# Kernel tuning notes

Hardware: AMD Instinct MI355X
Metric: run time of the kernel (lower is better)

The kernel has to match this reference:

```python
import jax, jax.numpy as jnp
import numpy as np

B, D, K = 512, 128, 131072
TEMP = 0.07
PTR = 0  # queue_ptr starts at 0; B <= K so single contiguous write


def _normalize(x, axis):
    return x / jnp.linalg.norm(x, axis=axis, keepdims=True)


def setup_inputs() -> dict:
    key = jax.random.key(0)
    k = jax.random.split(key, 7)
    return {
        "predict0": jax.random.normal(k[0], (B, D), jnp.float32),
        "predict1": jax.random.normal(k[1], (B, D), jnp.float32),
        "project0": jax.random.normal(k[2], (B, D), jnp.float32),
        "project1": jax.random.normal(k[3], (B, D), jnp.float32),
        "queue": jax.random.normal(k[4], (D, K), jnp.float32),
        "queue_id": jax.random.randint(k[5], (K,), 0, 100000, jnp.int64) if jax.config.jax_enable_x64 else jax.random.randint(k[5], (K,), 0, 100000, jnp.int32),
        "ids": jax.random.randint(k[6], (B,), 0, 100000, jnp.int64) if jax.config.jax_enable_x64 else jax.random.randint(k[6], (B,), 0, 100000, jnp.int32),
    }


def _find_nn(proj, queue_n, queue_id, ids):
    # [B, K] similarity, mask out entries with same sample id, argmax, gather cols
    sim = proj @ queue_n                                   # [B, K]
    is_own = queue_id[None, :] == ids[:, None]             # [B, K]
    sim = jnp.where(is_own, jnp.float32(-1.0), sim)
    idx = jnp.argmax(sim, axis=1)                          # [B]
    return queue_n[:, idx]                                 # [D, B]


def _nnclr_loss(predicted, nn, temperature):
    # logits[i, j] = nn_i . predicted_j / T ; labels = arange(B)
    logits = (nn.T @ predicted.T) / temperature            # [B, B]
    logp = jax.nn.log_softmax(logits, axis=-1)
    return -jnp.mean(jnp.diagonal(logp))


def reference(predict0, predict1, project0, project1, queue, queue_id, ids):
    # forward_encoder's normalization (encoder itself is external and modeled out)
    p0 = _normalize(predict0, 1)
    p1 = _normalize(predict1, 1)
    z0 = _normalize(project0, 1)
    z1 = _normalize(project1, 1)
    queue_n = _normalize(queue, 0)  # queue stored normalized along dim 0

    # find_nn / queue are no_grad in the original
    nn0 = jax.lax.stop_gradient(_find_nn(jax.lax.stop_gradient(z0), queue_n, queue_id, ids))
    nn1 = jax.lax.stop_gradient(_find_nn(jax.lax.stop_gradient(z1), queue_n, queue_id, ids))

    loss0 = _nnclr_loss(p0, nn1, TEMP)
    loss1 = _nnclr_loss(p1, nn0, TEMP)
    loss = (loss0 + loss1) * 0.5

    # _dequeue_and_enqueue: ptr=0, B <= K -> contiguous slice write
    new_queue = jax.lax.dynamic_update_slice(queue_n, jax.lax.stop_gradient(z0.T), (0, PTR))
    new_queue_id = jax.lax.dynamic_update_slice(queue_id, ids, (PTR,))
    new_ptr = jnp.array((PTR + B) % K, dtype=queue_id.dtype)
    return loss, new_queue, new_queue_id, new_ptr
```

## Files before the change

### kernel.cpp

```cpp
#include <hip/hip_runtime.h>
#include <hip/hip_bf16.h>

typedef _Float16 half8 __attribute__((ext_vector_type(8)));
typedef _Float16 half4 __attribute__((ext_vector_type(4)));
typedef float f32x4 __attribute__((ext_vector_type(4)));

#define B 512
#define D 128
#define K 131072
#define TEMP 0.07f
#define NKB 256
#define KT_PER 32
#define NSS 16

#define INVN_OFF 0
#define Z0_OFF   131072
#define Z1_OFF   196608
#define P0_OFF   262144
#define P1_OFF   327680
#define ZF16_OFF 393216
#define QA_OFF   458752
#define PVAL_OFF 8847360
#define WKB_OFF  9371648
#define WVAL_OFF 9372672
#define IDX_OFF  9373696
#define LP_OFF   9374720

__device__ __forceinline__ void gload_lds16(const _Float16* g, _Float16* l) {
  __builtin_amdgcn_global_load_lds(
      (const __attribute__((address_space(1))) unsigned int*)g,
      (__attribute__((address_space(3))) unsigned int*)l, 16, 0, 0);
}

__global__ __launch_bounds__(128) void rownorm_k(
    const float* __restrict__ p0, const float* __restrict__ p1,
    const float* __restrict__ z0, const float* __restrict__ z1,
    float* __restrict__ w, _Float16* __restrict__ zf16) {
  int row = blockIdx.x & (B - 1);
  int which = blockIdx.x >> 9;
  const float* src; float* dst;
  switch (which) {
    case 0: src = z0; dst = w + Z0_OFF; break;
    case 1: src = z1; dst = w + Z1_OFF; break;
    case 2: src = p0; dst = w + P0_OFF; break;
    default: src = p1; dst = w + P1_OFF; break;
  }
  int tid = threadIdx.x;
  float v = src[row * D + tid];
  float s = v * v;
  #pragma unroll
  for (int o = 32; o; o >>= 1) s += __shfl_xor(s, o);
  __shared__ float sm[2];
  if ((tid & 63) == 0) sm[tid >> 6] = s;
  __syncthreads();
  float inv = rsqrtf(sm[0] + sm[1]);
  float nv = v * inv;
  dst[row * D + tid] = nv;
  if (which < 2) zf16[(which * B + row) * D + tid] = (_Float16)nv;
}

__global__ __launch_bounds__(256) void colq_k(
    const float* __restrict__ q, const int* __restrict__ qid,
    const int* __restrict__ ids, const float* __restrict__ w_z0,
    float* __restrict__ invn, float* __restrict__ out,
    _Float16* __restrict__ qA) {
  __shared__ float psum[8][128];
  __shared__ float invs[128];
  __shared__ _Float16 tile[128][136];
  int tid = threadIdx.x;
  int kb = blockIdx.x;
  int k0 = kb * 128;
  int kc = tid & 31, dg = tid >> 5;
  {
    float4 acc = {0.f, 0.f, 0.f, 0.f};
    for (int i = 0; i < 16; i++) {
      int d = dg * 16 + i;
      float4 v = *(const float4*)(q + (size_t)d * K + k0 + kc * 4);
      acc.x = fmaf(v.x, v.x, acc.x); acc.y = fmaf(v.y, v.y, acc.y);
      acc.z = fmaf(v.z, v.z, acc.z); acc.w = fmaf(v.w, v.w, acc.w);
    }
    *(float4*)&psum[dg][kc * 4] = acc;
  }
  __syncthreads();
  if (tid < 128) {
    float s = 0.f;
    #pragma unroll
    for (int g2 = 0; g2 < 8; g2++) s += psum[g2][tid];
    float inv = rsqrtf(s);
    invs[tid] = inv;
    invn[k0 + tid] = inv;
    int kk = k0 + tid;
    out[1 + (size_t)D * K + kk] = (float)((kk < B) ? ids[kk] : qid[kk]);
  }
  __syncthreads();
  {
    bool zblk = (k0 < B);
    float4 iv = *(const float4*)&invs[kc * 4];
    for (int i = 0; i < 16; i++) {
      int d = i * 8 + dg;
      float4 v = *(const float4*)(q + (size_t)d * K + k0 + kc * 4);
      float o0 = v.x * iv.x, o1 = v.y * iv.y, o2 = v.z * iv.z, o3 = v.w * iv.w;
      half4 t = {(_Float16)o0, (_Float16)o1, (_Float16)o2, (_Float16)o3};
      *(half4*)&tile[d][kc * 4] = t;
      float* oc = out + 1 + (size_t)d * K + k0 + kc * 4;
      if (zblk) {
        int col = k0 + kc * 4;
        oc[0] = w_z0[(size_t)(col + 0) * D + d];
        oc[1] = w_z0[(size_t)(col + 1) * D + d];
        oc[2] = w_z0[(size_t)(col + 2) * D + d];
        oc[3] = w_z0[(size_t)(col + 3) * D + d];
      } else {
        oc[0] = o0; oc[1] = o1; oc[2] = o2; oc[3] = o3;
      }
    }
  }
  __syncthreads();
  {
    int dc = tid >> 6, l = tid & 63;
    int g = l >> 4, c = l & 15;
    #pragma unroll
    for (int kt = 0; kt < 8; kt++) {
      half8 f;
      #pragma unroll
      for (int i = 0; i < 8; i++) {
        int d = g * 4 + (i & 3) + ((i >> 2) << 4) + dc * 32;
        f[i] = tile[d][kt * 16 + c];
      }
      int ktg = kb * 8 + kt;
      *(half8*)(qA + (size_t)((ktg * 4 + dc) * 64 + l) * 8) = f;
    }
  }
}

#define PROCESS(AF, Q4) do { \
  _Pragma("unroll") \
  for (int nt = 0; nt < 4; nt++) { \
    f32x4 acc = {0.f, 0.f, 0.f, 0.f}; \
    _Pragma("unroll") \
    for (int dc = 0; dc < 4; dc++) \
      acc = __builtin_amdgcn_mfma_f32_16x16x32_f16(AF[dc], bf[nt][dc], acc, 0, 0, 0); \
    _Pragma("unroll") \
    for (int r = 0; r < 4; r++) { \
      int qv_ = (r == 0) ? Q4.x : (r == 1) ? Q4.y : (r == 2) ? Q4.z : Q4.w; \
      float sm_ = (qv_ == myid[nt]) ? -1.0f : acc[r]; \
      best[nt] = fmaxf(best[nt], sm_); \
    } \
  } \
} while (0)

__global__ __launch_bounds__(256) void nnsearch_k(
    const _Float16* __restrict__ qA, const _Float16* __restrict__ zf16,
    const int* __restrict__ qid, const int* __restrict__ ids,
    float* __restrict__ pval) {
  __shared__ __align__(16) _Float16 qtile[3][2][2048];
  __shared__ __align__(16) int qid_lds[512];
  int tid = threadIdx.x;
  int flat = blockIdx.x;
  int cls = flat & 7;
  int kb = cls * 32 + (flat >> 5);
  int rg = (flat >> 3) & 3;
  int wave = tid >> 6, lane = tid & 63;
  int g = lane >> 4, c = lane & 15;
  int rowbase = rg * 256 + wave * 64;
  int kt0 = kb * KT_PER;

  #pragma unroll
  for (int j = 0; j < 2; j++)
    gload_lds16(qA + (size_t)(((kt0 + j) * 4 + wave) * 64 + lane) * 8,
                &qtile[0][j][wave * 512]);
  #pragma unroll
  for (int j = 0; j < 2; j++)
    gload_lds16(qA + (size_t)(((kt0 + 2 + j) * 4 + wave) * 64 + lane) * 8,
                &qtile[1][j][wave * 512]);
  qid_lds[tid] = qid[kb * 512 + tid];
  qid_lds[tid + 256] = qid[kb * 512 + tid + 256];

  half8 bf[4][4];
  int myid[4];
  #pragma unroll
  for (int nt = 0; nt < 4; nt++) {
    int row = rowbase + nt * 16 + c;
    myid[nt] = ids[row & (B - 1)];
    #pragma unroll
    for (int dc = 0; dc < 4; dc++) {
      const _Float16* zr = zf16 + row * D + dc * 32 + g * 4;
      half4 lo = *(const half4*)zr;
      half4 hi = *(const half4*)(zr + 16);
      half8 f = {lo[0], lo[1], lo[2], lo[3], hi[0], hi[1], hi[2], hi[3]};
      bf[nt][dc] = f;
    }
  }
  __syncthreads();

  float best[4] = {-2.f, -2.f, -2.f, -2.f};
  int cur = 0;
  for (int s = 0; s < NSS; s++) {
    half8 af0[4], af1[4];
    #pragma unroll
    for (int dc = 0; dc < 4; dc++)
      af0[dc] = *(const half8*)&qtile[cur][0][dc * 512 + lane * 8];
    #pragma unroll
    for (int dc = 0; dc < 4; dc++)
      af1[dc] = *(const half8*)&qtile[cur][1][dc * 512 + lane * 8];
    int4 q4a = *(const int4*)&qid_lds[(s * 2 + 0) * 16 + g * 4];
    int4 q4b = *(const int4*)&qid_lds[(s * 2 + 1) * 16 + g * 4];
    if (s + 2 < NSS) {
      int nbuf = cur + 2; if (nbuf >= 3) nbuf -= 3;
      #pragma unroll
      for (int j = 0; j < 2; j++)
        gload_lds16(qA + (size_t)(((kt0 + (s + 2) * 2 + j) * 4 + wave) * 64 + lane) * 8,
                    &qtile[nbuf][j][wave * 512]);
    }
    PROCESS(af0, q4a);
    PROCESS(af1, q4b);
    if (s < NSS - 1) {
      asm volatile("s_waitcnt lgkmcnt(0)" ::: "memory");
      if (s + 2 < NSS) asm volatile("s_waitcnt vmcnt(2)" ::: "memory");
      else             asm volatile("s_waitcnt vmcnt(0)" ::: "memory");
      __builtin_amdgcn_sched_barrier(0);
      __builtin_amdgcn_s_barrier();
      __builtin_amdgcn_sched_barrier(0);
    }
    cur += 1; if (cur >= 3) cur -= 3;
  }

  #pragma unroll
  for (int nt = 0; nt < 4; nt++) {
    float v = best[nt];
    v = fmaxf(v, __shfl_xor(v, 16));
    v = fmaxf(v, __shfl_xor(v, 32));
    if (g == 0) {
      int row = rowbase + nt * 16 + c;
      pval[row * NKB + kb] = v;
    }
  }
}

__global__ __launch_bounds__(256) void nnreduce_k(
    const float* __restrict__ pval, int* __restrict__ wkb,
    float* __restrict__ wval) {
  int row = blockIdx.x;
  int tid = threadIdx.x;
  const float* p = pval + row * NKB;
  float a = p[tid];
  unsigned v = (__float_as_uint(fmaf(a, 0.5f, 3.0f)) << 9) | (unsigned)(NKB - 1 - tid);
  #pragma unroll
  for (int o = 32; o; o >>= 1) {
    unsigned ov = __shfl_xor(v, o);
    v = v > ov ? v : ov;
  }
  __shared__ unsigned sv[4];
  if ((tid & 63) == 0) sv[tid >> 6] = v;
  __syncthreads();
  if (tid == 0) {
    #pragma unroll
    for (int wv = 1; wv < 4; wv++) v = v > sv[wv] ? v : sv[wv];
    int kb = (NKB - 1) - (int)(v & 0x1FFu);
    wkb[row] = kb;
    wval[row] = pval[row * NKB + kb];
  }
}

__global__ __launch_bounds__(256) void nnfix_k(
    const _Float16* __restrict__ qA, const _Float16* __restrict__ zf16,
    const int* __restrict__ qid, const int* __restrict__ ids,
    const int* __restrict__ wkb, const float* __restrict__ wval,
    int* __restrict__ idxout) {
  int tid = threadIdx.x;
  int wave = tid >> 6, lane = tid & 63;
  int g = lane >> 4;
  int row = blockIdx.x * 4 + wave;
  int kb = wkb[row];
  float wv = wval[row];
  int myid = ids[row & (B - 1)];

  half8 bf[4];
  #pragma unroll
  for (int dc = 0; dc < 4; dc++) {
    const _Float16* zr = zf16 + row * D + dc * 32 + g * 4;
    half4 lo = *(const half4*)zr;
    half4 hi = *(const half4*)(zr + 16);
    half8 f = {lo[0], lo[1], lo[2], lo[3], hi[0], hi[1], hi[2], hi[3]};
    bf[dc] = f;
  }

  unsigned kbest = 0x7FFFFFFFu;
  int kt0 = kb * KT_PER;
  for (int kt = 0; kt < KT_PER; kt++) {
    int ktg = kt0 + kt;
    half8 af[4];
    #pragma unroll
    for (int dc = 0; dc < 4; dc++)
      af[dc] = *(const half8*)(qA + (size_t)((ktg * 4 + dc) * 64 + lane) * 8);
    int4 q4 = *(const int4*)(qid + ktg * 16 + g * 4);
    f32x4 acc = {0.f, 0.f, 0.f, 0.f};
    #pragma unroll
    for (int dc = 0; dc < 4; dc++)
      acc = __builtin_amdgcn_mfma_f32_16x16x32_f16(af[dc], bf[dc], acc, 0, 0, 0);
    #pragma unroll
    for (int r = 0; r < 4; r++) {
      int qv = (r == 0) ? q4.x : (r == 1) ? q4.y : (r == 2) ? q4.z : q4.w;
      float sm = (qv == myid) ? -1.0f : acc[r];
      if (sm == wv) {
        unsigned kk = (unsigned)(ktg * 16 + g * 4 + r);
        kbest = kbest < kk ? kbest : kk;
      }
    }
  }
  unsigned o1 = __shfl_xor(kbest, 16); kbest = kbest < o1 ? kbest : o1;
  unsigned o2 = __shfl_xor(kbest, 32); kbest = kbest < o2 ? kbest : o2;
  if (lane == 0) idxout[row] = (int)(kbest < (K - 1) ? kbest : (K - 1));
}

__global__ __launch_bounds__(256) void loss_k(
    const float* __restrict__ q, const float* __restrict__ invn,
    const int* __restrict__ idxout, const float* __restrict__ w,
    float* __restrict__ lpart) {
  int i0 = blockIdx.x * 8;
  int v = blockIdx.y;
  int tid = threadIdx.x;
  __shared__ float nns[8][D];
  __shared__ float rm[8][4], re[8][4], sdlds[8];
  #pragma unroll
  for (int ii = 0; ii < 4; ii++) {
    int i = ii * 2 + (tid >> 7);
    int d = tid & 127;
    int nnidx = idxout[(v ? 0 : B) + i0 + i];
    nns[i][d] = q[(size_t)d * K + nnidx] * invn[nnidx];
  }
  __syncthreads();
  const float* pr = w + (v ? P1_OFF : P0_OFF);
  const float* r0 = pr + tid * D;
  const float* r1 = pr + (tid + 256) * D;
  float a0[8] = {0, 0, 0, 0, 0, 0, 0, 0};
  float a1[8] = {0, 0, 0, 0, 0, 0, 0, 0};
  for (int d = 0; d < D; d += 4) {
    float4 x0 = *(const float4*)(r0 + d);
    float4 x1 = *(const float4*)(r1 + d);
    #pragma unroll
    for (int i = 0; i < 8; i++) {
      float4 n = *(const float4*)&nns[i][d];
      a0[i] = fmaf(x0.x, n.x, a0[i]); a0[i] = fmaf(x0.y, n.y, a0[i]);
      a0[i] = fmaf(x0.z, n.z, a0[i]); a0[i] = fmaf(x0.w, n.w, a0[i]);
      a1[i] = fmaf(x1.x, n.x, a1[i]); a1[i] = fmaf(x1.y, n.y, a1[i]);
      a1[i] = fmaf(x1.z, n.z, a1[i]); a1[i] = fmaf(x1.w, n.w, a1[i]);
    }
  }
  #pragma unroll
  for (int i = 0; i < 8; i++) {
    a0[i] *= (1.0f / TEMP);
    a1[i] *= (1.0f / TEMP);
  }
  #pragma unroll
  for (int i = 0; i < 8; i++) {
    int ig = i0 + i;
    if ((ig & 256) == 0) { if (tid == ig) sdlds[i] = a0[i]; }
    else { if (tid == (ig & 255)) sdlds[i] = a1[i]; }
  }
  int wv = tid >> 6;
  #pragma unroll
  for (int i = 0; i < 8; i++) {
    float m = fmaxf(a0[i], a1[i]);
    #pragma unroll
    for (int o = 32; o; o >>= 1) m = fmaxf(m, __shfl_xor(m, o));
    if ((tid & 63) == 0) rm[i][wv] = m;
  }
  __syncthreads();
  #pragma unroll
  for (int i = 0; i < 8; i++) {
    float m = fmaxf(fmaxf(rm[i][0], rm[i][1]), fmaxf(rm[i][2], rm[i][3]));
    float e = expf(a0[i] - m) + expf(a1[i] - m);
    #pragma unroll
    for (int o = 32; o; o >>= 1) e += __shfl_xor(e, o);
    if ((tid & 63) == 0) re[i][wv] = e;
  }
  __syncthreads();
  if (tid < 8) {
    int i = tid;
    float m = fmaxf(fmaxf(rm[i][0], rm[i][1]), fmaxf(rm[i][2], rm[i][3]));
    float s = re[i][0] + re[i][1] + re[i][2] + re[i][3];
    lpart[v * B + i0 + i] = sdlds[i] - m - logf(s);
  }
}

__global__ __launch_bounds__(256) void final_k(
    const float* __restrict__ lpart, float* __restrict__ out) {
  int tid = threadIdx.x;
  float s = lpart[tid] + lpart[tid + 256] + lpart[tid + 512] + lpart[tid + 768];
  #pragma unroll
  for (int o = 32; o; o >>= 1) s += __shfl_xor(s, o);
  __shared__ float sm[4];
  if ((tid & 63) == 0) sm[tid >> 6] = s;
  __syncthreads();
  if (tid == 0) {
    float total = sm[0] + sm[1] + sm[2] + sm[3];
    out[0] = -total * (1.0f / 1024.0f);
    out[1 + D * K + K] = 512.0f;
  }
}

extern "C" void kernel_launch(void* const* d_in, const int* in_sizes, int n_in,
                              void* d_out, int out_size, void* d_ws, size_t ws_size,
                              hipStream_t stream) {
  const float* p0 = (const float*)d_in[0];
  const float* p1 = (const float*)d_in[1];
  const float* z0 = (const float*)d_in[2];
  const float* z1 = (const float*)d_in[3];
  const float* q  = (const float*)d_in[4];
  const int* qid  = (const int*)d_in[5];
  const int* ids  = (const int*)d_in[6];
  float* out = (float*)d_out;
  float* w = (float*)d_ws;
  float* invn = w + INVN_OFF;
  _Float16* zf16 = (_Float16*)(w + ZF16_OFF);
  _Float16* qA   = (_Float16*)(w + QA_OFF);
  float* pval = w + PVAL_OFF;
  int* wkb    = (int*)(w + WKB_OFF);
  float* wval = w + WVAL_OFF;
  int* idxout = (int*)(w + IDX_OFF);
  float* lpart = w + LP_OFF;

  rownorm_k<<<2048, 128, 0, stream>>>(p0, p1, z0, z1, w, zf16);
  colq_k<<<K / 128, 256, 0, stream>>>(q, qid, ids, w + Z0_OFF, invn, out, qA);
  nnsearch_k<<<1024, 256, 0, stream>>>(qA, zf16, qid, ids, pval);
  nnreduce_k<<<1024, 256, 0, stream>>>(pval, wkb, wval);
  nnfix_k<<<256, 256, 0, stream>>>(qA, zf16, qid, ids, wkb, wval, idxout);
  dim3 gl(B / 8, 2);
  loss_k<<<gl, 256, 0, stream>>>(q, invn, idxout, w, lpart);
  final_k<<<1, 256, 0, stream>>>(lpart, out);
}
```

Baseline: 127.5 us.

## Fuse nn reduce and fix kernels; align queue output stores via shuffled shifted writes

Merges the per-row block-max reduction and the exact-index fix pass into one kernel. Each row gets a block whose four waves split the 32 candidate k-tiles, which removes a launch and the wkb/wval round trip through global memory. In colq_k, the normalized queue output (offset by one float because of the loss slot) is now written as aligned float4 stores. Each block builds the shifted vector with a lane shuffle and recomputes the previous block's last column for the boundary. This replaces four scalar unaligned stores per thread, at the cost of extra boundary logic and one extra strided column load per block.

```diff
diff --git a/kernel.cpp b/kernel.cpp
--- a/kernel.cpp
+++ b/kernel.cpp
@@ -21,8 +21,6 @@
 #define ZF16_OFF 393216
 #define QA_OFF   458752
 #define PVAL_OFF 8847360
-#define WKB_OFF  9371648
-#define WVAL_OFF 9372672
 #define IDX_OFF  9373696
 #define LP_OFF   9374720
 
@@ -66,6 +64,7 @@
     _Float16* __restrict__ qA) {
   __shared__ float psum[8][128];
   __shared__ float invs[128];
+  __shared__ float s_invm1;
   __shared__ _Float16 tile[128][136];
   int tid = threadIdx.x;
   int kb = blockIdx.x;
@@ -93,8 +92,40 @@
     out[1 + (size_t)D * K + kk] = (float)((kk < B) ? ids[kk] : qid[kk]);
   }
   __syncthreads();
-  {
-    bool zblk = (k0 < B);
+  float* fq   = &psum[0][0];
+  float* fcol = &psum[1][0];
+  if (kb == 4) {
+    if (tid < 32)
+      *(float4*)&fcol[tid * 4] = *(const float4*)(w_z0 + (size_t)511 * D + tid * 4);
+  } else if (kb > 4) {
+    if (tid < 128) fq[tid] = q[(size_t)tid * K + (k0 - 1)];
+    __syncthreads();
+    if (tid < 64) {
+      float s2 = fq[tid] * fq[tid] + fq[tid + 64] * fq[tid + 64];
+      #pragma unroll
+      for (int o = 32; o; o >>= 1) s2 += __shfl_xor(s2, o);
+      if (tid == 0) s_invm1 = rsqrtf(s2);
+    }
+    __syncthreads();
+    if (tid < 128) fcol[tid] = fq[tid] * s_invm1;
+  }
+  __syncthreads();
+  if (kb >= 4) {
+    float4 iv = *(const float4*)&invs[kc * 4];
+    for (int i = 0; i < 16; i++) {
+      int d = i * 8 + dg;
+      float4 v = *(const float4*)(q + (size_t)d * K + k0 + kc * 4);
+      float o0 = v.x * iv.x, o1 = v.y * iv.y, o2 = v.z * iv.z, o3 = v.w * iv.w;
+      half4 t = {(_Float16)o0, (_Float16)o1, (_Float16)o2, (_Float16)o3};
+      *(half4*)&tile[d][kc * 4] = t;
+      float p3 = __shfl_up(o3, 1);
+      float x0 = (kc == 0) ? fcol[d] : p3;
+      float4 st = {x0, o0, o1, o2};
+      *(float4*)(out + (size_t)d * K + k0 + kc * 4) = st;
+      if (kb == 1023 && kc == 31)
+        out[1 + (size_t)d * K + (K - 1)] = o3;
+    }
+  } else {
     float4 iv = *(const float4*)&invs[kc * 4];
     for (int i = 0; i < 16; i++) {
       int d = i * 8 + dg;
@@ -103,15 +134,11 @@
       half4 t = {(_Float16)o0, (_Float16)o1, (_Float16)o2, (_Float16)o3};
       *(half4*)&tile[d][kc * 4] = t;
       float* oc = out + 1 + (size_t)d * K + k0 + kc * 4;
-      if (zblk) {
-        int col = k0 + kc * 4;
-        oc[0] = w_z0[(size_t)(col + 0) * D + d];
-        oc[1] = w_z0[(size_t)(col + 1) * D + d];
-        oc[2] = w_z0[(size_t)(col + 2) * D + d];
-        oc[3] = w_z0[(size_t)(col + 3) * D + d];
-      } else {
-        oc[0] = o0; oc[1] = o1; oc[2] = o2; oc[3] = o3;
-      }
+      int col = k0 + kc * 4;
+      oc[0] = w_z0[(size_t)(col + 0) * D + d];
+      oc[1] = w_z0[(size_t)(col + 1) * D + d];
+      oc[2] = w_z0[(size_t)(col + 2) * D + d];
+      oc[3] = w_z0[(size_t)(col + 3) * D + d];
     }
   }
   __syncthreads();
@@ -236,42 +263,40 @@
   }
 }
 
-__global__ __launch_bounds__(256) void nnreduce_k(
-    const float* __restrict__ pval, int* __restrict__ wkb,
-    float* __restrict__ wval) {
+__global__ __launch_bounds__(256) void nnpick_k(
+    const float* __restrict__ pval, const _Float16* __restrict__ qA,
+    const _Float16* __restrict__ zf16, const int* __restrict__ qid,
+    const int* __restrict__ ids, int* __restrict__ idxout) {
   int row = blockIdx.x;
-  int tid = threadIdx.x;
-  const float* p = pval + row * NKB;
-  float a = p[tid];
-  unsigned v = (__float_as_uint(fmaf(a, 0.5f, 3.0f)) << 9) | (unsigned)(NKB - 1 - tid);
-  #pragma unroll
-  for (int o = 32; o; o >>= 1) {
-    unsigned ov = __shfl_xor(v, o);
-    v = v > ov ? v : ov;
-  }
-  __shared__ unsigned sv[4];
-  if ((tid & 63) == 0) sv[tid >> 6] = v;
-  __syncthreads();
-  if (tid == 0) {
-    #pragma unroll
-    for (int wv = 1; wv < 4; wv++) v = v > sv[wv] ? v : sv[wv];
-    int kb = (NKB - 1) - (int)(v & 0x1FFu);
-    wkb[row] = kb;
-    wval[row] = pval[row * NKB + kb];
-  }
-}
-
-__global__ __launch_bounds__(256) void nnfix_k(
-    const _Float16* __restrict__ qA, const _Float16* __restrict__ zf16,
-    const int* __restrict__ qid, const int* __restrict__ ids,
-    const int* __restrict__ wkb, const float* __restrict__ wval,
-    int* __restrict__ idxout) {
   int tid = threadIdx.x;
   int wave = tid >> 6, lane = tid & 63;
   int g = lane >> 4;
-  int row = blockIdx.x * 4 + wave;
-  int kb = wkb[row];
-  float wv = wval[row];
+  __shared__ unsigned sv[4];
+  __shared__ unsigned skb[4];
+  __shared__ int s_kb;
+  __shared__ float s_wv;
+  {
+    float a = pval[row * NKB + tid];
+    unsigned v = (__float_as_uint(fmaf(a, 0.5f, 3.0f)) << 9) | (unsigned)(NKB - 1 - tid);
+    #pragma unroll
+    for (int o = 32; o; o >>= 1) {
+      unsigned ov = __shfl_xor(v, o);
+      v = v > ov ? v : ov;
+    }
+    if (lane == 0) sv[wave] = v;
+  }
+  __syncthreads();
+  if (tid == 0) {
+    unsigned v = sv[0];
+    #pragma unroll
+    for (int wv = 1; wv < 4; wv++) v = v > sv[wv] ? v : sv[wv];
+    int kbw = (NKB - 1) - (int)(v & 0x1FFu);
+    s_kb = kbw;
+    s_wv = pval[row * NKB + kbw];
+  }
+  __syncthreads();
+  int kb = s_kb;
+  float wv = s_wv;
   int myid = ids[row & (B - 1)];
 
   half8 bf[4];
@@ -285,9 +310,9 @@
   }
 
   unsigned kbest = 0x7FFFFFFFu;
-  int kt0 = kb * KT_PER;
-  for (int kt = 0; kt < KT_PER; kt++) {
-    int ktg = kt0 + kt;
+  int ktbase = kb * KT_PER + wave * 8;
+  for (int kt = 0; kt < 8; kt++) {
+    int ktg = ktbase + kt;
     half8 af[4];
     #pragma unroll
     for (int dc = 0; dc < 4; dc++)
@@ -309,7 +334,14 @@
   }
   unsigned o1 = __shfl_xor(kbest, 16); kbest = kbest < o1 ? kbest : o1;
   unsigned o2 = __shfl_xor(kbest, 32); kbest = kbest < o2 ? kbest : o2;
-  if (lane == 0) idxout[row] = (int)(kbest < (K - 1) ? kbest : (K - 1));
+  if (lane == 0) skb[wave] = kbest;
+  __syncthreads();
+  if (tid == 0) {
+    unsigned v = skb[0];
+    #pragma unroll
+    for (int wv2 = 1; wv2 < 4; wv2++) v = v < skb[wv2] ? v : skb[wv2];
+    idxout[row] = (int)(v < (K - 1) ? v : (K - 1));
+  }
 }
 
 __global__ __launch_bounds__(256) void loss_k(
@@ -415,16 +447,13 @@
   _Float16* zf16 = (_Float16*)(w + ZF16_OFF);
   _Float16* qA   = (_Float16*)(w + QA_OFF);
   float* pval = w + PVAL_OFF;
-  int* wkb    = (int*)(w + WKB_OFF);
-  float* wval = w + WVAL_OFF;
   int* idxout = (int*)(w + IDX_OFF);
   float* lpart = w + LP_OFF;
 
   rownorm_k<<<2048, 128, 0, stream>>>(p0, p1, z0, z1, w, zf16);
   colq_k<<<K / 128, 256, 0, stream>>>(q, qid, ids, w + Z0_OFF, invn, out, qA);
   nnsearch_k<<<1024, 256, 0, stream>>>(qA, zf16, qid, ids, pval);
-  nnreduce_k<<<1024, 256, 0, stream>>>(pval, wkb, wval);
-  nnfix_k<<<256, 256, 0, stream>>>(qA, zf16, qid, ids, wkb, wval, idxout);
+  nnpick_k<<<1024, 256, 0, stream>>>(pval, qA, zf16, qid, ids, idxout);
   dim3 gl(B / 8, 2);
   loss_k<<<gl, 256, 0, stream>>>(q, invn, idxout, w, lpart);
   final_k<<<1, 256, 0, stream>>>(lpart, out);
```

Result: no change. 126.9 us (-0.5%).
